# Kernel optimization log

Measured on AMD Instinct MI355X. Metric: run time of the kernel, lower is better.

The kernel has to match this reference:

```python
import jax, jax.numpy as jnp
import numpy as np

N, H, W = 8, 512, 512
C = 16
TEX = 1024
LEVELS = 4
SH_START = 3


def setup_inputs() -> dict:
    key = jax.random.key(0)
    ks = jax.random.split(key, 2 + LEVELS)
    d = {
        "uv_map": jax.random.uniform(ks[0], (N, H, W, 2), dtype=jnp.float32),
        "sh_basis_map": jax.random.normal(ks[1], (N, H, W, 9), dtype=jnp.float32),
    }
    for i in range(LEVELS):
        s = int(round(TEX / 2.0 ** i))
        d[f"tex{i}"] = jax.random.normal(ks[2 + i], (s, s, C), dtype=jnp.float32) * 0.05
    return d


def _grid_sample_bilinear(tex, uv):
    """torch.grid_sample(mode=bilinear, padding=zeros, align_corners=False),
    grid built as (2u-1, -(2v-1)). tex: [Ht,Wt,C]; uv: [N,H,W,2] in [0,1].
    Returns [N,H,W,C]."""
    Ht, Wt, _ = tex.shape
    gx = uv[..., 0] * 2.0 - 1.0
    gy = -(uv[..., 1] * 2.0 - 1.0)  # y flip from original code
    ix = ((gx + 1.0) * Wt - 1.0) * 0.5  # unnormalize, align_corners=False
    iy = ((gy + 1.0) * Ht - 1.0) * 0.5
    ix0 = jnp.floor(ix); iy0 = jnp.floor(iy)
    ix1 = ix0 + 1.0;     iy1 = iy0 + 1.0
    wx1 = ix - ix0; wx0 = 1.0 - wx1
    wy1 = iy - iy0; wy0 = 1.0 - wy1

    def gather(iyf, ixf):
        iyi = iyf.astype(jnp.int32)
        ixi = ixf.astype(jnp.int32)
        valid = ((iyi >= 0) & (iyi < Ht) & (ixi >= 0) & (ixi < Wt))
        v = tex[jnp.clip(iyi, 0, Ht - 1), jnp.clip(ixi, 0, Wt - 1)]  # [N,H,W,C]
        return v * valid[..., None].astype(tex.dtype)  # zeros padding

    out = (gather(iy0, ix0) * (wy0 * wx0)[..., None]
           + gather(iy0, ix1) * (wy0 * wx1)[..., None]
           + gather(iy1, ix0) * (wy1 * wx0)[..., None]
           + gather(iy1, ix1) * (wy1 * wx1)[..., None])
    return out


def reference(uv_map, sh_basis_map, tex0, tex1, tex2, tex3):
    # accumulate all mipmap levels sampled at the same uv grid
    out = _grid_sample_bilinear(tex0, uv_map)
    for tex in (tex1, tex2, tex3):
        out = out + _grid_sample_bilinear(tex, uv_map)
    # mask pixels where u == 0
    mask = (uv_map[..., 0] == 0.0)[..., None]
    out = jnp.where(mask, 0.0, out)
    # SH multiply on channels [SH_START : SH_START+9]
    out = jnp.concatenate(
        [out[..., :SH_START],
         out[..., SH_START:SH_START + 9] * sh_basis_map,
         out[..., SH_START + 9:]], axis=-1)
    return out.transpose(0, 3, 1, 2)  # [N, C, H, W]
```

## Files before the change

kernel.cpp:

```cpp
#include <hip/hip_runtime.h>

#define NB 8
#define H 512
#define W 512
#define HW (H * W)
#define C 16
#define NPIX (NB * HW)
#define SH_START 3

#define G 32
#define NBINS (G * G)
#define CAP 3072
#define DUMPSLOT (NBINS * CAP)

#define BS_BLOCKS 256
#define BS_THREADS 1024
#define PXB (NPIX / BS_BLOCKS)
#define KPT (PXB / BS_THREADS)

#define OFF_INTER  ((size_t)0)
#define OFF_UV     ((size_t)100663360)
#define OFF_SLOT   ((size_t)125829248)
#define OFF_CUR    ((size_t)134217856)
#define WS_NEED    ((size_t)134221952)

#define D0 0
#define D1 (1156 * 8)
#define D2 ((1156 + 324) * 8)
#define D3 ((1156 + 324 + 100) * 8)
#define LDS_DWORDS ((1156 + 324 + 100 + 36) * 8)

typedef float f32x4 __attribute__((ext_vector_type(4)));
typedef unsigned int u32x2 __attribute__((ext_vector_type(2)));

__device__ __forceinline__ int bin_of(float u, float v) {
    int bx = (int)(u * (float)G);
    int by = (int)(v * (float)G);
    bx = bx < 0 ? 0 : (bx > G - 1 ? G - 1 : bx);
    by = by < 0 ? 0 : (by > G - 1 ? G - 1 : by);
    return by * G + bx;
}

__device__ __forceinline__ unsigned int f2bf(float f) {
    unsigned int u = __float_as_uint(f);
    unsigned int r = (u + 0x7FFFu + ((u >> 16) & 1u)) >> 16;
    return r & 0xFFFFu;
}

__global__ __launch_bounds__(BS_THREADS) void binsort_kernel(const float* __restrict__ uv,
                                                             int* __restrict__ cur,
                                                             float2* __restrict__ uvr,
                                                             int* __restrict__ slotmap) {
    __shared__ f32x4 stage[PXB];
    __shared__ int h[NBINS];
    __shared__ int lstart[NBINS];
    __shared__ int gbase[NBINS];
    __shared__ int wsum[16];
    int tid = threadIdx.x;
    int wv = tid >> 6;
    int lane = tid & 63;
    int pbase = blockIdx.x * PXB;
    const float2* uv2 = reinterpret_cast<const float2*>(uv);

    float2 p[KPT];
    int bn[KPT];
    h[tid] = 0;
    __syncthreads();
#pragma unroll
    for (int k = 0; k < KPT; ++k) {
        p[k] = uv2[pbase + tid + k * BS_THREADS];
        bn[k] = bin_of(p[k].x, p[k].y);
        atomicAdd(&h[bn[k]], 1);
    }
    __syncthreads();
    int cnt = h[tid];
    gbase[tid] = atomicAdd(&cur[tid], cnt);
    int x = cnt;
#pragma unroll
    for (int off = 1; off < 64; off <<= 1) {
        int up = __shfl_up(x, off);
        if (lane >= off) x += up;
    }
    if (lane == 63) wsum[wv] = x;
    __syncthreads();
    if (wv == 0 && lane < 16) {
        int y = wsum[lane];
#pragma unroll
        for (int off = 1; off < 16; off <<= 1) {
            int up = __shfl_up(y, off);
            if (lane >= off) y += up;
        }
        wsum[lane] = y;
    }
    __syncthreads();
    int wbase = (wv > 0) ? wsum[wv - 1] : 0;
    lstart[tid] = wbase + x - cnt;
    h[tid] = 0;
    __syncthreads();
#pragma unroll
    for (int k = 0; k < KPT; ++k) {
        int b = bn[k];
        int r = atomicAdd(&h[b], 1);
        int ls = lstart[b] + r;
        int within = gbase[b] + r;
        int gs = (within < CAP) ? (b * CAP + within) : DUMPSLOT;
        slotmap[pbase + tid + k * BS_THREADS] = gs;
        f32x4 rec;
        rec.x = p[k].x;
        rec.y = p[k].y;
        rec.z = 0.0f;
        rec.w = __int_as_float(gs);
        stage[ls] = rec;
    }
    __syncthreads();
#pragma unroll
    for (int k = 0; k < KPT; ++k) {
        f32x4 rec = stage[tid + k * BS_THREADS];
        int gs = __float_as_int(rec.w);
        uvr[gs] = make_float2(rec.x, rec.y);
    }
}

template<int S, int N>
__device__ __forceinline__ void stage_mip_bf16(const float* __restrict__ t,
                                               unsigned int* __restrict__ lbase,
                                               int x0, int y0, int tid) {
    for (int i = tid; i < N * N * 4; i += 512) {
        int tx = i >> 2, ch = i & 3;
        int ly = tx / N, lx = tx - ly * N;
        int gy = y0 + ly, gx = x0 + lx;
        u32x2 d = {0u, 0u};
        if (gy >= 0 && gy < S && gx >= 0 && gx < S) {
            f32x4 val = *reinterpret_cast<const f32x4*>(t + ((size_t)(gy * S + gx)) * C + ch * 4);
            d.x = f2bf(val.x) | (f2bf(val.y) << 16);
            d.y = f2bf(val.z) | (f2bf(val.w) << 16);
        }
        *reinterpret_cast<u32x2*>(lbase + (ly * N + lx) * 8 + ch * 2) = d;
    }
}

#define BFL(x) __uint_as_float((x) << 16)
#define BFH(x) __uint_as_float((x) & 0xFFFF0000u)

template<int S, int N>
__device__ __forceinline__ void sample_mip_bf16(const unsigned int* __restrict__ lbase,
                                                int x0, int y0,
                                                float u, float v, int ch2, f32x4& acc) {
    float Sf = (float)S;
    float gx = u * 2.0f - 1.0f;
    float gy = -(v * 2.0f - 1.0f);
    float ix = ((gx + 1.0f) * Sf - 1.0f) * 0.5f;
    float iy = ((gy + 1.0f) * Sf - 1.0f) * 0.5f;
    float ix0f = floorf(ix);
    float iy0f = floorf(iy);
    float wx1 = ix - ix0f;
    float wy1 = iy - iy0f;
    float wx0 = 1.0f - wx1;
    float wy0 = 1.0f - wy1;
    int lx = (int)ix0f - x0;
    int ly = (int)iy0f - y0;
    const unsigned int* p = lbase + (ly * N + lx) * 8 + ch2;
    u32x2 d00 = *reinterpret_cast<const u32x2*>(p);
    u32x2 d01 = *reinterpret_cast<const u32x2*>(p + 8);
    u32x2 d10 = *reinterpret_cast<const u32x2*>(p + 8 * N);
    u32x2 d11 = *reinterpret_cast<const u32x2*>(p + 8 * N + 8);
    float w00 = wy0 * wx0, w01 = wy0 * wx1, w10 = wy1 * wx0, w11 = wy1 * wx1;
    acc.x = fmaf(BFL(d00.x), w00, acc.x);
    acc.y = fmaf(BFH(d00.x), w00, acc.y);
    acc.z = fmaf(BFL(d00.y), w00, acc.z);
    acc.w = fmaf(BFH(d00.y), w00, acc.w);
    acc.x = fmaf(BFL(d01.x), w01, acc.x);
    acc.y = fmaf(BFH(d01.x), w01, acc.y);
    acc.z = fmaf(BFL(d01.y), w01, acc.z);
    acc.w = fmaf(BFH(d01.y), w01, acc.w);
    acc.x = fmaf(BFL(d10.x), w10, acc.x);
    acc.y = fmaf(BFH(d10.x), w10, acc.y);
    acc.z = fmaf(BFL(d10.y), w10, acc.z);
    acc.w = fmaf(BFH(d10.y), w10, acc.w);
    acc.x = fmaf(BFL(d11.x), w11, acc.x);
    acc.y = fmaf(BFH(d11.x), w11, acc.y);
    acc.z = fmaf(BFL(d11.y), w11, acc.z);
    acc.w = fmaf(BFH(d11.y), w11, acc.w);
}

__global__ __launch_bounds__(512) void phaseA_kernel(
    const float2* __restrict__ uvr, const int* __restrict__ cur,
    const float* __restrict__ t0, const float* __restrict__ t1,
    const float* __restrict__ t2, const float* __restrict__ t3,
    unsigned int* __restrict__ inter) {
    __shared__ unsigned int lds[LDS_DWORDS];
    int blk = blockIdx.x;
    int bin = (blk & 7) * (NBINS / 8) + (blk >> 3);
    int bx = bin & (G - 1), by = bin >> 5;
    int tid = threadIdx.x;

    int cnt = cur[bin];
    if (cnt > CAP) cnt = CAP;
    int start = bin * CAP;

    const int x0_0 = bx * 32 - 1, y0_0 = 1024 - (by + 1) * 32 - 1;
    const int x0_1 = bx * 16 - 1, y0_1 = 512  - (by + 1) * 16 - 1;
    const int x0_2 = bx * 8  - 1, y0_2 = 256  - (by + 1) * 8  - 1;
    const int x0_3 = bx * 4  - 1, y0_3 = 128  - (by + 1) * 4  - 1;

    stage_mip_bf16<1024, 34>(t0, lds + D0, x0_0, y0_0, tid);
    stage_mip_bf16<512,  18>(t1, lds + D1, x0_1, y0_1, tid);
    stage_mip_bf16<256,  10>(t2, lds + D2, x0_2, y0_2, tid);
    stage_mip_bf16<128,   6>(t3, lds + D3, x0_3, y0_3, tid);
    __syncthreads();

    int wave = tid >> 6;
    int lane = tid & 63;
    int q    = lane >> 2;
    int chq  = lane & 3;
    int ch2  = chq * 2;

    if (cnt <= 0) return;

    int i0 = wave * 16;
    int cm1 = cnt - 1;
    int i = i0 + q;
    float2 ruv = uvr[start + (i < cm1 ? i : cm1)];
    while (i0 < cnt) {
        int ni0 = i0 + 8 * 16;
        float2 nuv = ruv;
        if (ni0 < cnt) {
            int ni = ni0 + q;
            nuv = uvr[start + (ni < cm1 ? ni : cm1)];
        }
        float u = ruv.x, v = ruv.y;

        f32x4 a0 = {0.0f, 0.0f, 0.0f, 0.0f};
        f32x4 a1 = {0.0f, 0.0f, 0.0f, 0.0f};
        f32x4 a2 = {0.0f, 0.0f, 0.0f, 0.0f};
        f32x4 a3 = {0.0f, 0.0f, 0.0f, 0.0f};
        sample_mip_bf16<1024, 34>(lds + D0, x0_0, y0_0, u, v, ch2, a0);
        sample_mip_bf16<512,  18>(lds + D1, x0_1, y0_1, u, v, ch2, a1);
        sample_mip_bf16<256,  10>(lds + D2, x0_2, y0_2, u, v, ch2, a2);
        sample_mip_bf16<128,   6>(lds + D3, x0_3, y0_3, u, v, ch2, a3);
        f32x4 acc = (a0 + a1) + (a2 + a3);

        if (u == 0.0f) acc = (f32x4){0.0f, 0.0f, 0.0f, 0.0f};

        if (i0 + q < cnt) {
            u32x2 pk;
            pk.x = f2bf(acc.x) | (f2bf(acc.y) << 16);
            pk.y = f2bf(acc.z) | (f2bf(acc.w) << 16);
            u32x2* op = reinterpret_cast<u32x2*>(inter) + (size_t)(start + i0 + q) * 4 + chq;
            *op = pk;
        }
        ruv = nuv;
        i0 = ni0;
    }
}

__global__ __launch_bounds__(256) void phaseB_kernel(const unsigned int* __restrict__ inter,
                                                     const int* __restrict__ slotmap,
                                                     const float* __restrict__ sh,
                                                     float* __restrict__ out) {
    __shared__ float shs[256 * 9];
    int base = blockIdx.x * 256;
    const float* shp = sh + (size_t)base * 9;
    for (int i = threadIdx.x; i < 256 * 9; i += 256) shs[i] = shp[i];
    __syncthreads();

    int pix = base + threadIdx.x;
    int slot = slotmap[pix];
    const uint4* ip = reinterpret_cast<const uint4*>(inter) + (size_t)slot * 2;
    uint4 a = ip[0];
    uint4 b = ip[1];
    float c0  = BFL(a.x), c1  = BFH(a.x), c2  = BFL(a.y), c3  = BFH(a.y);
    float c4  = BFL(a.z), c5  = BFH(a.z), c6  = BFL(a.w), c7  = BFH(a.w);
    float c8  = BFL(b.x), c9  = BFH(b.x), c10 = BFL(b.y), c11 = BFH(b.y);
    float c12 = BFL(b.z), c13 = BFH(b.z), c14 = BFL(b.w), c15 = BFH(b.w);
    const float* s = &shs[threadIdx.x * 9];
    c3  *= s[0];
    c4  *= s[1]; c5  *= s[2]; c6  *= s[3]; c7  *= s[4];
    c8  *= s[5]; c9  *= s[6]; c10 *= s[7]; c11 *= s[8];

    int n  = pix >> 18;
    int hw = pix & (HW - 1);
    float* op = out + (size_t)n * C * HW + hw;
    __builtin_nontemporal_store(c0,  op + 0 * HW);
    __builtin_nontemporal_store(c1,  op + 1 * HW);
    __builtin_nontemporal_store(c2,  op + 2 * HW);
    __builtin_nontemporal_store(c3,  op + 3 * HW);
    __builtin_nontemporal_store(c4,  op + 4 * HW);
    __builtin_nontemporal_store(c5,  op + 5 * HW);
    __builtin_nontemporal_store(c6,  op + 6 * HW);
    __builtin_nontemporal_store(c7,  op + 7 * HW);
    __builtin_nontemporal_store(c8,  op + (size_t)8 * HW);
    __builtin_nontemporal_store(c9,  op + (size_t)9 * HW);
    __builtin_nontemporal_store(c10, op + (size_t)10 * HW);
    __builtin_nontemporal_store(c11, op + (size_t)11 * HW);
    __builtin_nontemporal_store(c12, op + (size_t)12 * HW);
    __builtin_nontemporal_store(c13, op + (size_t)13 * HW);
    __builtin_nontemporal_store(c14, op + (size_t)14 * HW);
    __builtin_nontemporal_store(c15, op + (size_t)15 * HW);
}

__device__ __forceinline__ void tap(const float* __restrict__ t, int S, int iy, int ix,
                                    float w, float acc[C]) {
    if (iy >= 0 && iy < S && ix >= 0 && ix < S) {
        const float4* p = reinterpret_cast<const float4*>(t + ((size_t)iy * S + ix) * C);
        float4 q0 = p[0];
        float4 q1 = p[1];
        float4 q2 = p[2];
        float4 q3 = p[3];
        acc[0]  = fmaf(q0.x, w, acc[0]);
        acc[1]  = fmaf(q0.y, w, acc[1]);
        acc[2]  = fmaf(q0.z, w, acc[2]);
        acc[3]  = fmaf(q0.w, w, acc[3]);
        acc[4]  = fmaf(q1.x, w, acc[4]);
        acc[5]  = fmaf(q1.y, w, acc[5]);
        acc[6]  = fmaf(q1.z, w, acc[6]);
        acc[7]  = fmaf(q1.w, w, acc[7]);
        acc[8]  = fmaf(q2.x, w, acc[8]);
        acc[9]  = fmaf(q2.y, w, acc[9]);
        acc[10] = fmaf(q2.z, w, acc[10]);
        acc[11] = fmaf(q2.w, w, acc[11]);
        acc[12] = fmaf(q3.x, w, acc[12]);
        acc[13] = fmaf(q3.y, w, acc[13]);
        acc[14] = fmaf(q3.z, w, acc[14]);
        acc[15] = fmaf(q3.w, w, acc[15]);
    }
}

__device__ __forceinline__ void sample_level(const float* __restrict__ t, int S,
                                             float u, float v, float acc[C]) {
    float Sf = (float)S;
    float gx = u * 2.0f - 1.0f;
    float gy = -(v * 2.0f - 1.0f);
    float ix = ((gx + 1.0f) * Sf - 1.0f) * 0.5f;
    float iy = ((gy + 1.0f) * Sf - 1.0f) * 0.5f;
    float ix0f = floorf(ix);
    float iy0f = floorf(iy);
    float wx1 = ix - ix0f;
    float wy1 = iy - iy0f;
    float wx0 = 1.0f - wx1;
    float wy0 = 1.0f - wy1;
    int ix0 = (int)ix0f;
    int iy0 = (int)iy0f;
    tap(t, S, iy0,     ix0,     wy0 * wx0, acc);
    tap(t, S, iy0,     ix0 + 1, wy0 * wx1, acc);
    tap(t, S, iy0 + 1, ix0,     wy1 * wx0, acc);
    tap(t, S, iy0 + 1, ix0 + 1, wy1 * wx1, acc);
}

__global__ __launch_bounds__(256) void texmap_kernel(
    const float* __restrict__ uv, const float* __restrict__ sh,
    const float* __restrict__ t0, const float* __restrict__ t1,
    const float* __restrict__ t2, const float* __restrict__ t3,
    float* __restrict__ out) {
    int idx = blockIdx.x * 256 + threadIdx.x;
    if (idx >= NPIX) return;

    float2 uvv = *reinterpret_cast<const float2*>(uv + (size_t)idx * 2);
    float u = uvv.x;
    float v = uvv.y;

    float acc[C];
#pragma unroll
    for (int c = 0; c < C; ++c) acc[c] = 0.0f;

    sample_level(t0, 1024, u, v, acc);
    sample_level(t1, 512,  u, v, acc);
    sample_level(t2, 256,  u, v, acc);
    sample_level(t3, 128,  u, v, acc);

    if (u == 0.0f) {
#pragma unroll
        for (int c = 0; c < C; ++c) acc[c] = 0.0f;
    }

    const float* shp = sh + (size_t)idx * 9;
#pragma unroll
    for (int j = 0; j < 9; ++j) acc[SH_START + j] *= shp[j];

    int n  = idx >> 18;
    int hw = idx & (HW - 1);
    float* op = out + (size_t)n * C * HW + hw;
#pragma unroll
    for (int c = 0; c < C; ++c) {
        __builtin_nontemporal_store(acc[c], op + (size_t)c * HW);
    }
}

extern "C" void kernel_launch(void* const* d_in, const int* in_sizes, int n_in,
                              void* d_out, int out_size, void* d_ws, size_t ws_size,
                              hipStream_t stream) {
    const float* uv = (const float*)d_in[0];
    const float* sh = (const float*)d_in[1];
    const float* t0 = (const float*)d_in[2];
    const float* t1 = (const float*)d_in[3];
    const float* t2 = (const float*)d_in[4];
    const float* t3 = (const float*)d_in[5];
    float* out = (float*)d_out;

    if (ws_size < WS_NEED) {
        texmap_kernel<<<dim3((NPIX + 255) / 256), dim3(256), 0, stream>>>(
            uv, sh, t0, t1, t2, t3, out);
        return;
    }

    char* ws = (char*)d_ws;
    unsigned int* inter   = (unsigned int*)(ws + OFF_INTER);
    float2*       uvr     = (float2*)(ws + OFF_UV);
    int*          slotmap = (int*)(ws + OFF_SLOT);
    int*          cur     = (int*)(ws + OFF_CUR);

    (void)hipMemsetAsync(cur, 0, NBINS * sizeof(int), stream);
    binsort_kernel<<<dim3(BS_BLOCKS), dim3(BS_THREADS), 0, stream>>>(uv, cur, uvr, slotmap);
    phaseA_kernel<<<dim3(NBINS), dim3(512), 0, stream>>>(
        uvr, cur, t0, t1, t2, t3, inter);
    phaseB_kernel<<<dim3(NPIX / 256), dim3(256), 0, stream>>>(inter, slotmap, sh, out);
}
```

Baseline: 160.5 us.

## Give each thread a whole pixel in phaseA, XOR-swizzle LDS texels, reuse binsort ranks

Phase A now assigns one pixel per thread with all 16 channels, instead of four lanes sharing a pixel with four channels each. This removes the duplicated coordinate and weight math and allows 32-byte vector stores of the intermediate. The staged texture tiles use an XOR swizzle on channel quads by row, plus padding between mip levels, to cut LDS bank conflicts when a wave gathers random texels. The binsort kernel keeps the rank returned by the first histogram atomic, so the second atomic pass and the histogram reset are gone. Holding 16 accumulators per thread raises register pressure.

Measured after the change: 185.1 us. 15.4% more time.

```diff
diff --git a/kernel.cpp b/kernel.cpp
--- a/kernel.cpp
+++ b/kernel.cpp
@@ -24,11 +24,15 @@
 #define OFF_CUR    ((size_t)134217856)
 #define WS_NEED    ((size_t)134221952)
 
+#define SZ0 (1156 * 8 + 16)
+#define SZ1 (324 * 8 + 16)
+#define SZ2 (100 * 8 + 16)
+#define SZ3 (36 * 8 + 16)
 #define D0 0
-#define D1 (1156 * 8)
-#define D2 ((1156 + 324) * 8)
-#define D3 ((1156 + 324 + 100) * 8)
-#define LDS_DWORDS ((1156 + 324 + 100 + 36) * 8)
+#define D1 (D0 + SZ0)
+#define D2 (D1 + SZ1)
+#define D3 (D2 + SZ2)
+#define LDS_DWORDS (D3 + SZ3)
 
 typedef float f32x4 __attribute__((ext_vector_type(4)));
 typedef unsigned int u32x2 __attribute__((ext_vector_type(2)));
@@ -46,6 +50,9 @@
     unsigned int r = (u + 0x7FFFu + ((u >> 16) & 1u)) >> 16;
     return r & 0xFFFFu;
 }
+
+#define BFL(x) __uint_as_float((x) << 16)
+#define BFH(x) __uint_as_float((x) & 0xFFFF0000u)
 
 __global__ __launch_bounds__(BS_THREADS) void binsort_kernel(const float* __restrict__ uv,
                                                              int* __restrict__ cur,
@@ -64,13 +71,14 @@
 
     float2 p[KPT];
     int bn[KPT];
+    int rk[KPT];
     h[tid] = 0;
     __syncthreads();
 #pragma unroll
     for (int k = 0; k < KPT; ++k) {
         p[k] = uv2[pbase + tid + k * BS_THREADS];
         bn[k] = bin_of(p[k].x, p[k].y);
-        atomicAdd(&h[bn[k]], 1);
+        rk[k] = atomicAdd(&h[bn[k]], 1);
     }
     __syncthreads();
     int cnt = h[tid];
@@ -95,12 +103,11 @@
     __syncthreads();
     int wbase = (wv > 0) ? wsum[wv - 1] : 0;
     lstart[tid] = wbase + x - cnt;
-    h[tid] = 0;
     __syncthreads();
 #pragma unroll
     for (int k = 0; k < KPT; ++k) {
         int b = bn[k];
-        int r = atomicAdd(&h[b], 1);
+        int r = rk[k];
         int ls = lstart[b] + r;
         int within = gbase[b] + r;
         int gs = (within < CAP) ? (b * CAP + within) : DUMPSLOT;
@@ -135,22 +142,33 @@
             d.x = f2bf(val.x) | (f2bf(val.y) << 16);
             d.y = f2bf(val.z) | (f2bf(val.w) << 16);
         }
-        *reinterpret_cast<u32x2*>(lbase + (ly * N + lx) * 8 + ch * 2) = d;
-    }
-}
-
-#define BFL(x) __uint_as_float((x) << 16)
-#define BFH(x) __uint_as_float((x) & 0xFFFF0000u)
+        *reinterpret_cast<u32x2*>(lbase + tx * 8 + (((ch ^ (ly & 3)) & 3) << 1)) = d;
+    }
+}
+
+__device__ __forceinline__ void tap16s(const unsigned int* __restrict__ p, int s, float w,
+                                       f32x4& c0, f32x4& c1, f32x4& c2, f32x4& c3) {
+    u32x2 d0 = *reinterpret_cast<const u32x2*>(p + (((0 ^ s) & 3) << 1));
+    u32x2 d1 = *reinterpret_cast<const u32x2*>(p + (((1 ^ s) & 3) << 1));
+    u32x2 d2 = *reinterpret_cast<const u32x2*>(p + (((2 ^ s) & 3) << 1));
+    u32x2 d3 = *reinterpret_cast<const u32x2*>(p + (((3 ^ s) & 3) << 1));
+    c0.x = fmaf(BFL(d0.x), w, c0.x); c0.y = fmaf(BFH(d0.x), w, c0.y);
+    c0.z = fmaf(BFL(d0.y), w, c0.z); c0.w = fmaf(BFH(d0.y), w, c0.w);
+    c1.x = fmaf(BFL(d1.x), w, c1.x); c1.y = fmaf(BFH(d1.x), w, c1.y);
+    c1.z = fmaf(BFL(d1.y), w, c1.z); c1.w = fmaf(BFH(d1.y), w, c1.w);
+    c2.x = fmaf(BFL(d2.x), w, c2.x); c2.y = fmaf(BFH(d2.x), w, c2.y);
+    c2.z = fmaf(BFL(d2.y), w, c2.z); c2.w = fmaf(BFH(d2.y), w, c2.w);
+    c3.x = fmaf(BFL(d3.x), w, c3.x); c3.y = fmaf(BFH(d3.x), w, c3.y);
+    c3.z = fmaf(BFL(d3.y), w, c3.z); c3.w = fmaf(BFH(d3.y), w, c3.w);
+}
 
 template<int S, int N>
-__device__ __forceinline__ void sample_mip_bf16(const unsigned int* __restrict__ lbase,
-                                                int x0, int y0,
-                                                float u, float v, int ch2, f32x4& acc) {
+__device__ __forceinline__ void samp(const unsigned int* __restrict__ lbase,
+                                     int x0, int y0, float u, float v,
+                                     f32x4& c0, f32x4& c1, f32x4& c2, f32x4& c3) {
     float Sf = (float)S;
-    float gx = u * 2.0f - 1.0f;
-    float gy = -(v * 2.0f - 1.0f);
-    float ix = ((gx + 1.0f) * Sf - 1.0f) * 0.5f;
-    float iy = ((gy + 1.0f) * Sf - 1.0f) * 0.5f;
+    float ix = fmaf(u, Sf, -0.5f);
+    float iy = fmaf(-v, Sf, Sf - 0.5f);
     float ix0f = floorf(ix);
     float iy0f = floorf(iy);
     float wx1 = ix - ix0f;
@@ -159,28 +177,16 @@
     float wy0 = 1.0f - wy1;
     int lx = (int)ix0f - x0;
     int ly = (int)iy0f - y0;
-    const unsigned int* p = lbase + (ly * N + lx) * 8 + ch2;
-    u32x2 d00 = *reinterpret_cast<const u32x2*>(p);
-    u32x2 d01 = *reinterpret_cast<const u32x2*>(p + 8);
-    u32x2 d10 = *reinterpret_cast<const u32x2*>(p + 8 * N);
-    u32x2 d11 = *reinterpret_cast<const u32x2*>(p + 8 * N + 8);
+    int tb = ly * N + lx;
+    int s0 = ly & 3;
+    int s1 = (ly + 1) & 3;
+    const unsigned int* r0 = lbase + tb * 8;
+    const unsigned int* r1 = lbase + (tb + N) * 8;
     float w00 = wy0 * wx0, w01 = wy0 * wx1, w10 = wy1 * wx0, w11 = wy1 * wx1;
-    acc.x = fmaf(BFL(d00.x), w00, acc.x);
-    acc.y = fmaf(BFH(d00.x), w00, acc.y);
-    acc.z = fmaf(BFL(d00.y), w00, acc.z);
-    acc.w = fmaf(BFH(d00.y), w00, acc.w);
-    acc.x = fmaf(BFL(d01.x), w01, acc.x);
-    acc.y = fmaf(BFH(d01.x), w01, acc.y);
-    acc.z = fmaf(BFL(d01.y), w01, acc.z);
-    acc.w = fmaf(BFH(d01.y), w01, acc.w);
-    acc.x = fmaf(BFL(d10.x), w10, acc.x);
-    acc.y = fmaf(BFH(d10.x), w10, acc.y);
-    acc.z = fmaf(BFL(d10.y), w10, acc.z);
-    acc.w = fmaf(BFH(d10.y), w10, acc.w);
-    acc.x = fmaf(BFL(d11.x), w11, acc.x);
-    acc.y = fmaf(BFH(d11.x), w11, acc.y);
-    acc.z = fmaf(BFL(d11.y), w11, acc.z);
-    acc.w = fmaf(BFH(d11.y), w11, acc.w);
+    tap16s(r0,     s0, w00, c0, c1, c2, c3);
+    tap16s(r0 + 8, s0, w01, c0, c1, c2, c3);
+    tap16s(r1,     s1, w10, c0, c1, c2, c3);
+    tap16s(r1 + 8, s1, w11, c0, c1, c2, c3);
 }
 
 __global__ __launch_bounds__(512) void phaseA_kernel(
@@ -209,48 +215,54 @@
     stage_mip_bf16<128,   6>(t3, lds + D3, x0_3, y0_3, tid);
     __syncthreads();
 
+    if (cnt <= 0) return;
+
     int wave = tid >> 6;
     int lane = tid & 63;
-    int q    = lane >> 2;
-    int chq  = lane & 3;
-    int ch2  = chq * 2;
-
-    if (cnt <= 0) return;
-
-    int i0 = wave * 16;
     int cm1 = cnt - 1;
-    int i = i0 + q;
+
+    int i = wave * 64 + lane;
     float2 ruv = uvr[start + (i < cm1 ? i : cm1)];
-    while (i0 < cnt) {
-        int ni0 = i0 + 8 * 16;
+    while (i - lane < cnt) {
+        int ni = i + 512;
         float2 nuv = ruv;
-        if (ni0 < cnt) {
-            int ni = ni0 + q;
+        if (ni - lane < cnt) {
             nuv = uvr[start + (ni < cm1 ? ni : cm1)];
         }
         float u = ruv.x, v = ruv.y;
 
-        f32x4 a0 = {0.0f, 0.0f, 0.0f, 0.0f};
-        f32x4 a1 = {0.0f, 0.0f, 0.0f, 0.0f};
-        f32x4 a2 = {0.0f, 0.0f, 0.0f, 0.0f};
-        f32x4 a3 = {0.0f, 0.0f, 0.0f, 0.0f};
-        sample_mip_bf16<1024, 34>(lds + D0, x0_0, y0_0, u, v, ch2, a0);
-        sample_mip_bf16<512,  18>(lds + D1, x0_1, y0_1, u, v, ch2, a1);
-        sample_mip_bf16<256,  10>(lds + D2, x0_2, y0_2, u, v, ch2, a2);
-        sample_mip_bf16<128,   6>(lds + D3, x0_3, y0_3, u, v, ch2, a3);
-        f32x4 acc = (a0 + a1) + (a2 + a3);
-
-        if (u == 0.0f) acc = (f32x4){0.0f, 0.0f, 0.0f, 0.0f};
-
-        if (i0 + q < cnt) {
-            u32x2 pk;
-            pk.x = f2bf(acc.x) | (f2bf(acc.y) << 16);
-            pk.y = f2bf(acc.z) | (f2bf(acc.w) << 16);
-            u32x2* op = reinterpret_cast<u32x2*>(inter) + (size_t)(start + i0 + q) * 4 + chq;
-            *op = pk;
+        f32x4 c0 = {0.0f, 0.0f, 0.0f, 0.0f};
+        f32x4 c1 = {0.0f, 0.0f, 0.0f, 0.0f};
+        f32x4 c2 = {0.0f, 0.0f, 0.0f, 0.0f};
+        f32x4 c3 = {0.0f, 0.0f, 0.0f, 0.0f};
+        samp<1024, 34>(lds + D0, x0_0, y0_0, u, v, c0, c1, c2, c3);
+        samp<512,  18>(lds + D1, x0_1, y0_1, u, v, c0, c1, c2, c3);
+        samp<256,  10>(lds + D2, x0_2, y0_2, u, v, c0, c1, c2, c3);
+        samp<128,   6>(lds + D3, x0_3, y0_3, u, v, c0, c1, c2, c3);
+
+        if (u == 0.0f) {
+            c0 = (f32x4){0.0f, 0.0f, 0.0f, 0.0f};
+            c1 = (f32x4){0.0f, 0.0f, 0.0f, 0.0f};
+            c2 = (f32x4){0.0f, 0.0f, 0.0f, 0.0f};
+            c3 = (f32x4){0.0f, 0.0f, 0.0f, 0.0f};
+        }
+
+        if (i < cnt) {
+            uint4 lo, hi;
+            lo.x = f2bf(c0.x) | (f2bf(c0.y) << 16);
+            lo.y = f2bf(c0.z) | (f2bf(c0.w) << 16);
+            lo.z = f2bf(c1.x) | (f2bf(c1.y) << 16);
+            lo.w = f2bf(c1.z) | (f2bf(c1.w) << 16);
+            hi.x = f2bf(c2.x) | (f2bf(c2.y) << 16);
+            hi.y = f2bf(c2.z) | (f2bf(c2.w) << 16);
+            hi.z = f2bf(c3.x) | (f2bf(c3.y) << 16);
+            hi.w = f2bf(c3.z) | (f2bf(c3.w) << 16);
+            uint4* op = reinterpret_cast<uint4*>(inter) + (size_t)(start + i) * 2;
+            op[0] = lo;
+            op[1] = hi;
         }
         ruv = nuv;
-        i0 = ni0;
+        i = ni;
     }
 }
 
```
